# Kernel optimization log

Hardware: AMD Instinct MI355X
Metric: run time of the kernel (lower is better)

The kernel has to match this reference:

```python
import jax, jax.numpy as jnp
import numpy as np
from jax.scipy.special import logsumexp

N_LABELS = 64
BOS_INDEX = 0
B, S = 32, 512


def setup_inputs() -> dict:
    key = jax.random.key(0)
    k1, k2, k3 = jax.random.split(key, 3)
    emits = jax.random.normal(k1, (B, S, N_LABELS * N_LABELS), dtype=jnp.float32)
    targets = jax.random.randint(k2, (B, S + 1), 0, N_LABELS, dtype=jnp.int64)
    # mask: valid-prefix mask from random lengths in [2, S]
    lengths = jax.random.randint(k3, (B,), 2, S + 1)
    mask = (jnp.arange(S)[None, :] < lengths[:, None])
    return {"emits": emits, "targets": targets, "mask": mask}


def reference(emits, targets, mask):
    # emits: [B, S, L*L], targets: [B, S+1], mask: [B, S]; order=2 CRF NLL loss
    L = N_LABELS
    b, s, _ = emits.shape
    em = jnp.transpose(emits, (1, 0, 2))          # [S, B, L*L]
    tg = targets.T                                 # [S+1, B]
    mk = mask.T                                    # [S, B]

    em4 = em.reshape(s, b, L, L)                   # [S, B, prev, next]
    log_alpha0 = em4[0, :, BOS_INDEX, :]           # [B, L]

    def step(log_alpha, inp):
        e_i, m_i = inp                             # [B, L, L], [B]
        scores = log_alpha[:, :, None] + e_i       # [B, prev, next]
        new = logsumexp(scores, axis=1)            # [B, L]
        log_alpha = jnp.where(m_i[:, None], new, log_alpha)
        return log_alpha, None

    log_alpha, _ = jax.lax.scan(step, log_alpha0, (em4[1:], mk[1:]))
    log_z = logsumexp(log_alpha, axis=1).sum()

    # gold path score: pair index = prev_tag * L + next_tag
    idx = tg[:-1] * L + tg[1:]                     # [S, B]
    gold = jnp.take_along_axis(em, idx[:, :, None], axis=-1)[..., 0]  # [S, B]
    score = jnp.where(mk, gold, 0.0).sum()

    total_token = mk.sum().astype(emits.dtype)
    loss = (log_z - score) / total_token
    return loss
```

## Files before the change

### kernel.cpp

```cpp
#include <hip/hip_runtime.h>
#include <math.h>


constexpr int S_LEN   = 512;
constexpr int NB      = 32;
constexpr int NL      = 64;
constexpr int LL      = 4096;
constexpr int CL      = 16;
constexpr int NCH     = 32;
constexpr int NCHUNKS = NB * NCH;

#define LN2F 0.69314718055994531f
#define PREF 4.6588830833596715f

typedef _Float16 h4 __attribute__((ext_vector_type(4)));
typedef float    f4 __attribute__((ext_vector_type(4)));
union U4 { unsigned u[2]; h4 v; };

__device__ __forceinline__ float bl(float v, int sl) {
  return __int_as_float(__builtin_amdgcn_readlane(__float_as_int(v), sl));
}
__device__ __forceinline__ unsigned pk2(float a, float b) {
  auto r = __builtin_amdgcn_cvt_pkrtz(a, b);
  return __builtin_bit_cast(unsigned, r);
}
__device__ __forceinline__ float expw(float x) {
  return __expf(x - PREF);
}

__global__ __launch_bounds__(64) void crf_chunk(
    const float* __restrict__ emits,
    const int*   __restrict__ targets,
    const int*   __restrict__ mask,
    _Float16*    __restrict__ matP,
    float*       __restrict__ wsf)
{
  const int ci   = blockIdx.x;
  const int b    = ci >> 5;
  const int cc   = ci & 31;
  const int lane = threadIdx.x;
  const int c    = lane & 15;
  const int h    = lane >> 4;
  const float* __restrict__ eb = emits + (size_t)b * (S_LEN * LL);

  int len;
  {
    const int* mb = mask + b * S_LEN;
    int cnt = 0;
    #pragma unroll
    for (int i = 0; i < 8; ++i) cnt += (mb[i * 64 + lane] != 0);
    #pragma unroll
    for (int off = 32; off; off >>= 1) cnt += __shfl_xor(cnt, off);
    len = cnt;
  }

  {
    float g = 0.f;
    const int s = 16 * cc + (lane & 15);
    if (lane < 16 && s < len) {
      const int* tb = targets + b * (S_LEN + 1);
      g = eb[(size_t)s * LL + tb[s] * NL + tb[s + 1]];
    }
    #pragma unroll
    for (int off = 32; off; off >>= 1) g += __shfl_xor(g, off);
    if (lane == 0) wsf[NCHUNKS + ci] = g;
  }

  const int s0 = 16 * cc + 1;
  const int n  = min(len - s0, CL);
  if (n < 1) return;

  h4 bf[4][4];
  #pragma unroll
  for (int K = 0; K < 4; ++K)
    #pragma unroll
    for (int J = 0; J < 4; ++J) {
      h4 v;
      #pragma unroll
      for (int i = 0; i < 4; ++i)
        v[i] = (_Float16)((K == J && (4 * h + i) == c) ? 1.0f : 0.0f);
      bf[K][J] = v;
    }

  float Lacc = 0.f;
  f4 LB0[4][4], LB1[4][4];
  h4 af[4][4];

#define LOADE(LB, S)                                                         \
  do { const float* ep = eb + (size_t)(S) * LL;                              \
    _Pragma("unroll") for (int I = 0; I < 4; ++I) {                          \
      const float* rp = ep + (16 * I + c) * 64 + 4 * h;                      \
      _Pragma("unroll") for (int K = 0; K < 4; ++K)                          \
        LB[I][K] = *reinterpret_cast<const f4*>(rp + 16 * K);                \
    } } while (0)

#define BUILDAF(LB)                                                          \
  do { _Pragma("unroll") for (int I = 0; I < 4; ++I)                         \
    _Pragma("unroll") for (int K = 0; K < 4; ++K) {                          \
      U4 x;                                                                  \
      x.u[0] = pk2(expw(LB[I][K][0]), expw(LB[I][K][1]));                    \
      x.u[1] = pk2(expw(LB[I][K][2]), expw(LB[I][K][3]));                    \
      af[I][K] = x.v;                                                        \
    } } while (0)

#define STEPM(LBC, M)                                                        \
  do { if ((M) <= n) {                                                       \
    BUILDAF(LBC);                              \
    if ((M) + 2 <= n) LOADE(LBC, s0 + n - 2 - (M));    \
    const bool rn = ((((M) & 7) == 0) || ((M) == n));                        \
    float mh = 0.f;                                                          \
    {                                                \
      f4 dh[4][2];                                                           \
      _Pragma("unroll") for (int I = 0; I < 4; ++I)                          \
        _Pragma("unroll") for (int J = 0; J < 2; ++J) {                      \
          f4 d = {0.f, 0.f, 0.f, 0.f};                                       \
          _Pragma("unroll") for (int K = 0; K < 4; ++K)                      \
            d = __builtin_amdgcn_mfma_f32_16x16x16f16(af[I][K], bf[K][J], d, 0, 0, 0); \
          dh[I][J] = d;                                                      \
        }                                                                    \
      if (rn) {                                                              \
        _Pragma("unroll") for (int I = 0; I < 4; ++I)                        \
          _Pragma("unroll") for (int J = 0; J < 2; ++J)                      \
            _Pragma("unroll") for (int u = 0; u < 4; ++u)                    \
              mh = fmaxf(mh, dh[I][J][u]);                                   \
      }                                                                      \
      _Pragma("unroll") for (int K = 0; K < 4; ++K)                          \
        _Pragma("unroll") for (int J = 0; J < 2; ++J) {                      \
          U4 y;                                                              \
          y.u[0] = pk2(dh[K][J][0], dh[K][J][1]);                            \
          y.u[1] = pk2(dh[K][J][2], dh[K][J][3]);                            \
          bf[K][J] = y.v;                                                    \
        }                                                                    \
    }                                                                        \
    {                                                \
      f4 dh[4][2];                                                           \
      _Pragma("unroll") for (int I = 0; I < 4; ++I)                          \
        _Pragma("unroll") for (int J = 0; J < 2; ++J) {                      \
          f4 d = {0.f, 0.f, 0.f, 0.f};                                       \
          _Pragma("unroll") for (int K = 0; K < 4; ++K)                      \
            d = __builtin_amdgcn_mfma_f32_16x16x16f16(af[I][K], bf[K][J + 2], d, 0, 0, 0); \
          dh[I][J] = d;                                                      \
        }                                                                    \
      if (rn) {                                                              \
        _Pragma("unroll") for (int I = 0; I < 4; ++I)                        \
          _Pragma("unroll") for (int J = 0; J < 2; ++J)                      \
            _Pragma("unroll") for (int u = 0; u < 4; ++u)                    \
              mh = fmaxf(mh, dh[I][J][u]);                                   \
      }                                                                      \
      _Pragma("unroll") for (int K = 0; K < 4; ++K)                          \
        _Pragma("unroll") for (int J = 0; J < 2; ++J) {                      \
          U4 y;                                                              \
          y.u[0] = pk2(dh[K][J][0], dh[K][J][1]);                            \
          y.u[1] = pk2(dh[K][J][2], dh[K][J][3]);                            \
          bf[K][J + 2] = y.v;                                                \
        }                                                                    \
    }                                                                        \
    Lacc += PREF;                                                            \
    if (rn) {                                                                \
      _Pragma("unroll") for (int off = 32; off; off >>= 1)                   \
        mh = fmaxf(mh, __shfl_xor(mh, off));                                 \
      const int E = (__float_as_int(mh) >> 23) & 0xFF;                       \
      const _Float16 hs = (_Float16)__int_as_float((254 - E) << 23);         \
      const h4 hv = {hs, hs, hs, hs};                                        \
      _Pragma("unroll") for (int K = 0; K < 4; ++K)                          \
        _Pragma("unroll") for (int J = 0; J < 4; ++J) bf[K][J] *= hv;        \
      Lacc += (float)(E - 127) * LN2F;                                       \
    }                                                                        \
  } } while (0)

  LOADE(LB0, s0 + n - 1);
  if (n > 1) LOADE(LB1, s0 + n - 2);
  for (int m = 1; m <= n; m += 2) {
    STEPM(LB0, m);
    STEPM(LB1, m + 1);
  }

  {
    _Float16* mp = matP + (size_t)ci * 4096;
    #pragma unroll
    for (int I = 0; I < 4; ++I)
      #pragma unroll
      for (int J = 0; J < 4; ++J)
        #pragma unroll
        for (int i = 0; i < 4; ++i)
          mp[(I * 4 + J) * 256 + i * 64 + lane] = bf[I][J][i];
  }
  if (lane == 0) wsf[ci] = Lacc;
}

__global__ __launch_bounds__(64) void crf_fold(
    const float* __restrict__ emits,
    const int*   __restrict__ mask,
    const _Float16* __restrict__ matP,
    const float* __restrict__ wsf,
    float*       __restrict__ wso,
    int*         __restrict__ done,
    float*       __restrict__ out)
{
  const int b = blockIdx.x, lane = threadIdx.x;
  const int c = lane & 15, h = lane >> 4;
  const float* __restrict__ eb = emits + (size_t)b * (S_LEN * LL);

  int len;
  {
    const int* mb = mask + b * S_LEN;
    int cnt = 0;
    #pragma unroll
    for (int i = 0; i < 8; ++i) cnt += (mb[i * 64 + lane] != 0);
    #pragma unroll
    for (int off = 32; off; off >>= 1) cnt += __shfl_xor(cnt, off);
    len = cnt;
  }
  const int nact = (len + 14) >> 4;

  const bool on = (c == 0);
  const h4 HZ = {(_Float16)0, (_Float16)0, (_Float16)0, (_Float16)0};

  float la[16];
  #pragma unroll
  for (int K = 0; K < 4; ++K)
    #pragma unroll
    for (int i = 0; i < 4; ++i) la[K * 4 + i] = eb[16 * K + 4 * h + i];
  float mm = la[0];
  #pragma unroll
  for (int i = 1; i < 16; ++i) mm = fmaxf(mm, la[i]);
  const float m0 = fmaxf(fmaxf(bl(mm, 0), bl(mm, 16)), fmaxf(bl(mm, 32), bl(mm, 48)));
  float Lacc = m0;
  h4 bv[4];
  #pragma unroll
  for (int K = 0; K < 4; ++K) {
    U4 y;
    y.u[0] = pk2(__expf(la[4 * K] - m0), __expf(la[4 * K + 1] - m0));
    y.u[1] = pk2(__expf(la[4 * K + 2] - m0), __expf(la[4 * K + 3] - m0));
    bv[K] = on ? y.v : HZ;
  }

  h4 A0[4][4], A1[4][4];

#define LOADA(AF, CH)                                                        \
  do { const _Float16* mp = matP + (size_t)(b * NCH + (CH)) * 4096;          \
    _Pragma("unroll") for (int I = 0; I < 4; ++I)                            \
      _Pragma("unroll") for (int K = 0; K < 4; ++K)                          \
        AF[I][K] = *reinterpret_cast<const h4*>(                             \
            mp + (I * 4 + K) * 256 + (c & 3) * 64 + 16 * (c >> 2) + 4 * h);  \
  } while (0)

#define FOLD(AF, CH)                                                         \
  do { f4 dv[4];                                                             \
    _Pragma("unroll") for (int I = 0; I < 4; ++I) {                          \
      f4 d = {0.f, 0.f, 0.f, 0.f};                                           \
      _Pragma("unroll") for (int K = 0; K < 4; ++K)                          \
        d = __builtin_amdgcn_mfma_f32_16x16x16f16(AF[I][K], bv[K], d, 0, 0, 0); \
      dv[I] = d;                                                             \
    }                                                                        \
    float mx = dv[0][0];                                                     \
    _Pragma("unroll") for (int I = 0; I < 4; ++I)                            \
      _Pragma("unroll") for (int u = 0; u < 4; ++u) mx = fmaxf(mx, dv[I][u]); \
    float gm;                                                                \
    if (((CH) & 3) == 3) {                                                   \
      gm = fmaxf(fmaxf(bl(mx, 0), bl(mx, 16)),                               \
                 fmaxf(bl(mx, 32), bl(mx, 48)));                             \
    } else {                                                                 \
      gm = bl(mx, 0);                                                        \
    }                                                                        \
    const int E = (__float_as_int(gm) >> 23) & 0xFF;                         \
    const float scale = __int_as_float((254 - E) << 23);                     \
    Lacc += (float)(E - 127) * LN2F + wsf[b * NCH + (CH)];                   \
    _Pragma("unroll") for (int I = 0; I < 4; ++I) {                          \
      U4 y;                                                                  \
      y.u[0] = pk2(dv[I][0] * scale, dv[I][1] * scale);                      \
      y.u[1] = pk2(dv[I][2] * scale, dv[I][3] * scale);                      \
      bv[I] = on ? y.v : HZ;                                                 \
    } } while (0)

  LOADA(A0, 0);
  for (int ch = 0; ch < nact; ++ch) {
    if (ch & 1) { if (ch + 1 < nact) LOADA(A0, ch + 1); FOLD(A1, ch); }
    else        { if (ch + 1 < nact) LOADA(A1, ch + 1); FOLD(A0, ch); }
  }

  float qs = 0.f;
  #pragma unroll
  for (int K = 0; K < 4; ++K)
    #pragma unroll
    for (int i = 0; i < 4; ++i) qs += (float)bv[K][i];
  const float q0 = (bl(qs, 0) + bl(qs, 16)) + (bl(qs, 32) + bl(qs, 48));
  if (lane == 0) {
    wso[b]      = Lacc + __logf(q0);
    wso[32 + b] = (float)len;
  }

  __threadfence();
  int isLast = 0;
  if (lane == 0) isLast = (atomicAdd(done, 1) == NB - 1);
  isLast = __shfl(isLast, 0);
  if (isLast) {
    __threadfence();
    const float* gold = wsf + NCHUNKS;
    float gs = 0.f;
    #pragma unroll
    for (int i = 0; i < NCHUNKS / 64; ++i) gs += gold[i * 64 + lane];
    float lz = (lane < NB) ? wso[lane] : 0.f;
    float ln = (lane < NB) ? wso[32 + lane] : 0.f;
    #pragma unroll
    for (int off = 32; off; off >>= 1) {
      gs += __shfl_xor(gs, off);
      lz += __shfl_xor(lz, off);
      ln += __shfl_xor(ln, off);
    }
    if (lane == 0) out[0] = (lz - gs) / ln;
  }
}

extern "C" void kernel_launch(void* const* d_in, const int* in_sizes, int n_in,
                              void* d_out, int out_size, void* d_ws, size_t ws_size,
                              hipStream_t stream) {
  const float* emits   = (const float*)d_in[0];
  const int*   targets = (const int*)d_in[1];
  const int*   mask    = (const int*)d_in[2];
  float* out = (float*)d_out;

  _Float16* matP = (_Float16*)d_ws;
  float*    wsf  = (float*)((char*)d_ws + (size_t)NCHUNKS * 4096 * 2);
  float*    wso  = wsf + 2 * NCHUNKS;
  int*      done = (int*)(wso + 64);

  hipMemsetAsync(done, 0, sizeof(int), stream);
  hipLaunchKernelGGL(crf_chunk, dim3(NCHUNKS), dim3(64), 0, stream,
                     emits, targets, mask, matP, wsf);
  hipLaunchKernelGGL(crf_fold, dim3(NB), dim3(64), 0, stream,
                     emits, mask, matP, wsf, wso, done, out);
}
```

Measured before the change: 77.80 us.

## Stage emission tiles via global_load_lds into a swizzled LDS double buffer

Replaces the register-held double buffer of emission tiles (two sets of 16 float4 per lane) with direct global-to-LDS async loads into a two-slot shared ring. The ring uses an XOR swizzle to avoid bank conflicts, and explicit vmcnt/lgkmcnt waits plus sched barriers control the overlap. The aim is to cut VGPR pressure and keep the prefetch of the next step in flight during the MFMA recurrence. The cost is LDS traffic, 32KB of LDS per block, and fragile hand-written waitcnt logic.

After: 75.08 us. -3.5%, faster.

```diff
diff --git a/kernel.cpp b/kernel.cpp
--- a/kernel.cpp
+++ b/kernel.cpp
@@ -27,6 +27,11 @@
 __device__ __forceinline__ float expw(float x) {
   return __expf(x - PREF);
 }
+__device__ __forceinline__ void gld16(const void* g, void* l) {
+  __builtin_amdgcn_global_load_lds(
+      (const __attribute__((address_space(1))) unsigned*)g,
+      (__attribute__((address_space(3))) unsigned*)l, 16, 0, 0);
+}
 
 __global__ __launch_bounds__(64) void crf_chunk(
     const float* __restrict__ emits,
@@ -35,6 +40,8 @@
     _Float16*    __restrict__ matP,
     float*       __restrict__ wsf)
 {
+  __shared__ float ring[2][4096];
+
   const int ci   = blockIdx.x;
   const int b    = ci >> 5;
   const int cc   = ci & 31;
@@ -70,6 +77,16 @@
   const int n  = min(len - s0, CL);
   if (n < 1) return;
 
+  const int pe = h * 256 + ((c ^ h) * 16);
+  const int po = h * 256 + ((c ^ (h + 4)) * 16);
+
+#define STAGE(SLOT, S)                                                       \
+  do { const char* mbase = (const char*)(eb + (size_t)(S) * LL);             \
+    char* lbase = (char*)&ring[SLOT][0];                                     \
+    _Pragma("unroll") for (int q = 0; q < 16; ++q) {                         \
+      gld16(mbase + q * 1024 + ((q & 1) ? po : pe), lbase + q * 1024);       \
+    } } while (0)
+
   h4 bf[4][4];
   #pragma unroll
   for (int K = 0; K < 4; ++K)
@@ -83,30 +100,29 @@
     }
 
   float Lacc = 0.f;
-  f4 LB0[4][4], LB1[4][4];
   h4 af[4][4];
 
-#define LOADE(LB, S)                                                         \
-  do { const float* ep = eb + (size_t)(S) * LL;                              \
-    _Pragma("unroll") for (int I = 0; I < 4; ++I) {                          \
-      const float* rp = ep + (16 * I + c) * 64 + 4 * h;                      \
-      _Pragma("unroll") for (int K = 0; K < 4; ++K)                          \
-        LB[I][K] = *reinterpret_cast<const f4*>(rp + 16 * K);                \
-    } } while (0)
-
-#define BUILDAF(LB)                                                          \
-  do { _Pragma("unroll") for (int I = 0; I < 4; ++I)                         \
-    _Pragma("unroll") for (int K = 0; K < 4; ++K) {                          \
-      U4 x;                                                                  \
-      x.u[0] = pk2(expw(LB[I][K][0]), expw(LB[I][K][1]));                    \
-      x.u[1] = pk2(expw(LB[I][K][2]), expw(LB[I][K][3]));                    \
-      af[I][K] = x.v;                                                        \
-    } } while (0)
-
-#define STEPM(LBC, M)                                                        \
+#define BUILDAF(SLOT)                                                        \
+  do { const char* Wb = (const char*)&ring[SLOT][0];                         \
+    _Pragma("unroll") for (int I = 0; I < 4; ++I)                            \
+      _Pragma("unroll") for (int K = 0; K < 4; ++K) {                        \
+        f4 t = *(const f4*)(Wb + (16 * I + c) * 256 +                        \
+                            (((4 * K + h) ^ (c & 7)) * 16));                 \
+        U4 x;                                                                \
+        x.u[0] = pk2(expw(t[0]), expw(t[1]));                                \
+        x.u[1] = pk2(expw(t[2]), expw(t[3]));                                \
+        af[I][K] = x.v;                                                      \
+      } } while (0)
+
+#define STEPM(M)                                                             \
   do { if ((M) <= n) {                                                       \
-    BUILDAF(LBC);                              \
-    if ((M) + 2 <= n) LOADE(LBC, s0 + n - 2 - (M));    \
+    if ((M) == n) { asm volatile("s_waitcnt vmcnt(0)" ::: "memory"); }       \
+    else          { asm volatile("s_waitcnt vmcnt(16)" ::: "memory"); }      \
+    __builtin_amdgcn_sched_barrier(0);                                       \
+    BUILDAF(((M) - 1) & 1);                                                  \
+    asm volatile("s_waitcnt lgkmcnt(0)" ::: "memory");    \
+    __builtin_amdgcn_sched_barrier(0);                                       \
+    if ((M) + 2 <= n) STAGE(((M) - 1) & 1, s0 + n - 2 - (M));                \
     const bool rn = ((((M) & 7) == 0) || ((M) == n));                        \
     float mh = 0.f;                                                          \
     {                                                \
@@ -168,11 +184,11 @@
     }                                                                        \
   } } while (0)
 
-  LOADE(LB0, s0 + n - 1);
-  if (n > 1) LOADE(LB1, s0 + n - 2);
+  STAGE(0, s0 + n - 1);
+  if (n > 1) STAGE(1, s0 + n - 2);
   for (int m = 1; m <= n; m += 2) {
-    STEPM(LB0, m);
-    STEPM(LB1, m + 1);
+    STEPM(m);
+    STEPM(m + 1);
   }
 
   {
```
